# Performance work log

Hardware: AMD Instinct MI355X
Metric: run time of the kernel (lower is better)

Reference implementation:

```python
import jax, jax.numpy as jnp
import numpy as np

K_SPLINE = 3
GRID_N = 3
NUM_BASIS = GRID_N + K_SPLINE  # 6 coefficients per spline edge


def _make_grid(in_dim):
    # pykan-style uniform grid on [-1, 1] extended by k knots each side
    h = 2.0 / GRID_N
    g = -1.0 + h * jnp.arange(-K_SPLINE, GRID_N + K_SPLINE + 1, dtype=jnp.float32)
    return jnp.broadcast_to(g, (in_dim, g.shape[0]))  # [in, G+2k+1]


def _b_splines(x, grid):
    # Cox-de Boor recursion. x: [N, in], grid: [in, G+2k+1] -> [N, in, G+k]
    x = x[:, :, None]
    g = grid[None, :, :]
    B = ((x >= g[:, :, :-1]) & (x < g[:, :, 1:])).astype(x.dtype)
    for p in range(1, K_SPLINE + 1):
        B = ((x - g[:, :, :-(p + 1)]) / (g[:, :, p:-1] - g[:, :, :-(p + 1)]) * B[:, :, :-1]
             + (g[:, :, p + 1:] - x) / (g[:, :, p + 1:] - g[:, :, 1:-p]) * B[:, :, 1:])
    return B


def _kan_layer(x, grid, coef, scale_base, scale_sp, bias):
    # KANLayer: out_j = sum_i scale_base[i,j]*silu(x_i) + scale_sp[i,j]*spline_ij(x_i) + bias_j
    B = _b_splines(x, grid)                              # [N, in, G+k]
    spline = jnp.einsum('nib,iob->nio', B, coef)         # [N, in, out]
    act = scale_base[None] * jax.nn.silu(x)[:, :, None] + scale_sp[None] * spline
    return act.sum(axis=1) + bias[None, :]


def _calculate_w(strain, params):
    # strain: [B, S, 3] -> W: [B, S, 1]
    s1, s2, s3 = strain[..., 0], strain[..., 1], strain[..., 2]
    # C = 2E + I with E = [[s1, s3/2], [s3/2, s2]]
    a = 2.0 * s1 + 1.0
    d = 2.0 * s2 + 1.0
    b = s3
    detC = a * d - b * b
    logJ = 0.5 * jnp.log(detC)                           # log(det(C)**0.5)
    # analytic eigvalsh of symmetric 2x2, ascending order; double-where keeps
    # gradients finite at the degenerate point (strain == 0, C == I)
    m = 0.5 * (a + d)
    h2 = 0.25 * (a - d) ** 2 + b * b
    r = jnp.where(h2 > 0, jnp.sqrt(jnp.where(h2 > 0, h2, 1.0)), 0.0)
    eigs = jnp.sqrt(jnp.stack([m - r, m + r], axis=-1))  # principal stretches [B,S,2]
    aux = detC ** (-1.0 / 6.0)                           # J**(-1/3)
    reg = eigs * aux[..., None]
    kan_in = jnp.concatenate([reg ** params['ki0'],
                              (logJ * params['ki1'])[..., None]], axis=-1)  # [B,S,3]
    Bn, Sn = kan_in.shape[0], kan_in.shape[1]
    flat = kan_in.reshape(Bn * Sn, 3)
    h = _kan_layer(flat, _make_grid(3), params['coef0'], params['sb0'], params['sp0'], params['b0'])
    out = _kan_layer(h, _make_grid(1), params['coef1'], params['sb1'], params['sp1'], params['b1'])
    return out.reshape(Bn, Sn, -1)


def _forward(strain, params):
    # grad of sum(W) wrt strain (grad_outputs = ones), minus the same grad at zero strain.
    gradW = jax.grad(lambda s: _calculate_w(s, params).sum())(strain)
    zeros = jnp.zeros((1, 1, 3), strain.dtype)           # grad at 0 is identical per element
    grad0 = jax.grad(lambda s: _calculate_w(s, params).sum())(zeros)
    return gradW - grad0


def setup_inputs() -> dict:
    key = jax.random.key(0)
    ks = jax.random.split(key, 4)
    B, S = 4096, 512
    strain = 0.1 * jax.random.uniform(ks[0], (B, S, 3), dtype=jnp.float32)
    coef0 = 0.1 * jax.random.normal(ks[1], (3, 1, NUM_BASIS), dtype=jnp.float32)
    coef1 = 0.1 * jax.random.normal(ks[2], (1, 1, NUM_BASIS), dtype=jnp.float32)
    return {
        'strain': strain,
        'coef0': coef0,
        'sb0': jnp.full((3, 1), 1.0 / np.sqrt(3.0), jnp.float32),
        'sp0': jnp.ones((3, 1), jnp.float32),
        'b0': jnp.zeros((1,), jnp.float32),
        'coef1': coef1,
        'sb1': jnp.ones((1, 1), jnp.float32),
        'sp1': jnp.ones((1, 1), jnp.float32),
        'b1': jnp.zeros((1,), jnp.float32),
        'ki0': jnp.asarray(1.37, jnp.float32),  # ki[0] = 1 + random()
        'ki1': jnp.asarray(1.0, jnp.float32),   # ki[-1] fixed to 1.0 in __init__
    }


def reference(strain, coef0, sb0, sp0, b0, coef1, sb1, sp1, b1, ki0, ki1):
    params = {'coef0': coef0, 'sb0': sb0, 'sp0': sp0, 'b0': b0,
              'coef1': coef1, 'sb1': sb1, 'sp1': sp1, 'b1': b1,
              'ki0': ki0, 'ki1': ki1}
    return _forward(strain, params)
```

## Files before the change

kernel.cpp:

```cpp
#include <hip/hip_runtime.h>
#include <math.h>

#define NB 6

struct Params {
    float sb0[3], sp0[3];
    float b0;
    float sb1, sp1;
    float ki0, ki1;
};

__device__ __forceinline__ float fexp2(float x) { return __builtin_amdgcn_exp2f(x); }
__device__ __forceinline__ float flog2(float x) { return __builtin_amdgcn_logf(x); }
__device__ __forceinline__ float frcp(float x)  { return __builtin_amdgcn_rcpf(x); }
__device__ __forceinline__ float frsq(float x)  { return __builtin_amdgcn_rsqf(x); }

__device__ __forceinline__ void spline_eval(float x, const float (*__restrict__ tab)[8],
                                            float& sp, float& dsp) {
    float u  = fmaf(x, 1.5f, 4.5f);
    float fi = floorf(u);
    float f  = u - fi;
    int   i  = (int)fi;
    float msk = (u >= 0.0f && u < 9.0f) ? 1.0f : 0.0f;
    i = i < 0 ? 0 : (i > 8 ? 8 : i);
    const float4 A  = *reinterpret_cast<const float4*>(&tab[i][0]);
    const float4 Bv = *reinterpret_cast<const float4*>(&tab[i][4]);
    sp  = msk * fmaf(fmaf(fmaf(A.w, f, A.z), f, A.y), f, A.x);
    dsp = msk * fmaf(fmaf(Bv.z, f, Bv.y), f, Bv.x);
}

__device__ __forceinline__ void silu_fd(float x, float& s, float& ds) {
    float e   = fexp2(-1.44269504f * x);
    float sig = frcp(1.0f + e);
    s  = x * sig;
    ds = sig * (1.0f + x * (1.0f - sig));
}

__device__ void grad_sample(float s1, float s2, float s3, const Params& P,
                            const float (*__restrict__ tab)[9][8], float g[3]) {
    float a   = fmaf(2.0f, s1, 1.0f);
    float d   = fmaf(2.0f, s2, 1.0f);
    float b   = s3;
    float m   = 0.5f * (a + d);
    float amd = a - d;
    float h2  = fmaf(0.25f * amd, amd, b * b);
    bool  pos = h2 > 0.0f;
    float irr = pos ? frsq(h2) : 0.0f;
    float r   = h2 * irr;
    float t1  = m - r, t2 = m + r;
    float invDet = frcp(t1 * t2);
    float invt1 = t2 * invDet, invt2 = t1 * invDet;
    float Lt1 = flog2(t1), Lt2 = flog2(t2);
    float k   = P.ki0;
    float x0  = fexp2(k * (Lt1 * (1.0f / 3.0f) - Lt2 * (1.0f / 6.0f)));
    float x1  = fexp2(k * (Lt2 * (1.0f / 3.0f) - Lt1 * (1.0f / 6.0f)));
    float x2  = P.ki1 * 0.34657359f * (Lt1 + Lt2);

    float xs[3] = {x0, x1, x2};
    float hacc  = P.b0;
    float gx[3];
#pragma unroll
    for (int i = 0; i < 3; ++i) {
        float sp, dsp;
        spline_eval(xs[i], tab[i], sp, dsp);
        float si, dsi; silu_fd(xs[i], si, dsi);
        hacc += P.sb0[i] * si + P.sp0[i] * sp;
        gx[i] = P.sb0[i] * dsi + P.sp0[i] * dsp;
    }
    float sp2, dsp2;
    spline_eval(hacc, tab[3], sp2, dsp2);
    float si2, dsi2; silu_fd(hacc, si2, dsi2);
    float dWdh = P.sb1 * dsi2 + P.sp1 * dsp2;

    float P0 = dWdh * gx[0] * x0 * k;
    float P1 = dWdh * gx[1] * x1 * k;
    float w2c = dWdh * gx[2];
    float A = 0.5f * P0 * invt1;
    float B = 0.5f * P1 * invt2;
    float C = invDet * (0.5f * P.ki1 * w2c - (P0 + P1) * (1.0f / 6.0f));
    float dr0 = 0.25f * amd * irr;
    float dr2 = b * irr;
    float ApB = A + B, BmA = B - A;
    float h05 = 0.5f * ApB;
    float gA = h05 + BmA * dr0 + C * d;
    float gD = h05 - BmA * dr0 + C * a;
    float gB = BmA * dr2 - 2.0f * b * C;
    g[0] = 2.0f * gA;
    g[1] = 2.0f * gD;
    g[2] = gB;
}

__global__ __launch_bounds__(256) void kan_grad(
        const float* __restrict__ strain, float* __restrict__ out, int n,
        const float* __restrict__ c0, const float* __restrict__ sb0,
        const float* __restrict__ sp0, const float* __restrict__ b0,
        const float* __restrict__ c1, const float* __restrict__ sb1,
        const float* __restrict__ sp1, const float* __restrict__ ki0,
        const float* __restrict__ ki1) {
    __shared__ float tab[4][9][8];
    __shared__ float g0s[3];

    const int t = threadIdx.x;
    if (t < 36) {
        int tbl = t / 9, cell = t % 9;
        const float* cp = (tbl < 3) ? (c0 + tbl * NB) : c1;
        float cv[4];
#pragma unroll
        for (int kk = 0; kk < 4; ++kk) {
            int j = cell + kk - 3;
            cv[kk] = (j >= 0 && j < NB) ? cp[j] : 0.0f;
        }
        const float c16 = 1.0f / 6.0f;
        float a0 = (cv[0] + 4.0f * cv[1] + cv[2]) * c16;
        float a1 = (cv[2] - cv[0]) * 0.5f;
        float a2 = (cv[0] - 2.0f * cv[1] + cv[2]) * 0.5f;
        float a3 = (cv[3] - cv[0] + 3.0f * (cv[1] - cv[2])) * c16;
        tab[tbl][cell][0] = a0;
        tab[tbl][cell][1] = a1;
        tab[tbl][cell][2] = a2;
        tab[tbl][cell][3] = a3;
        tab[tbl][cell][4] = 1.5f * a1;
        tab[tbl][cell][5] = 3.0f * a2;
        tab[tbl][cell][6] = 4.5f * a3;
        tab[tbl][cell][7] = 0.0f;
    }

    Params P;
#pragma unroll
    for (int i = 0; i < 3; ++i) { P.sb0[i] = sb0[i]; P.sp0[i] = sp0[i]; }
    P.b0 = b0[0];
    P.sb1 = sb1[0]; P.sp1 = sp1[0];
    P.ki0 = ki0[0]; P.ki1 = ki1[0];

    __syncthreads();
    if (t == 0) {
        float g0[3];
        grad_sample(0.0f, 0.0f, 0.0f, P, tab, g0);
        g0s[0] = g0[0]; g0s[1] = g0[1]; g0s[2] = g0[2];
    }
    __syncthreads();
    const float g00 = g0s[0], g01 = g0s[1], g02 = g0s[2];

    const int ngroups = (n + 3) >> 2;
    for (int gi = blockIdx.x * blockDim.x + threadIdx.x; gi < ngroups;
         gi += gridDim.x * blockDim.x) {
        int i0 = gi * 4;
        if (i0 + 4 <= n) {
            const float4* sp4 = reinterpret_cast<const float4*>(strain + (size_t)i0 * 3);
            float4 v0 = sp4[0], v1 = sp4[1], v2 = sp4[2];
            float in[12] = {v0.x, v0.y, v0.z, v0.w,
                            v1.x, v1.y, v1.z, v1.w,
                            v2.x, v2.y, v2.z, v2.w};
            float o[12];
#pragma unroll
            for (int kk = 0; kk < 4; ++kk) {
                float g[3];
                grad_sample(in[3 * kk], in[3 * kk + 1], in[3 * kk + 2], P, tab, g);
                o[3 * kk]     = g[0] - g00;
                o[3 * kk + 1] = g[1] - g01;
                o[3 * kk + 2] = g[2] - g02;
            }
            float4* op4 = reinterpret_cast<float4*>(out + (size_t)i0 * 3);
            op4[0] = make_float4(o[0], o[1], o[2],  o[3]);
            op4[1] = make_float4(o[4], o[5], o[6],  o[7]);
            op4[2] = make_float4(o[8], o[9], o[10], o[11]);
        } else {
            for (int i = i0; i < n; ++i) {
                float g[3];
                grad_sample(strain[3 * i], strain[3 * i + 1], strain[3 * i + 2], P,
                            tab, g);
                out[3 * i]     = g[0] - g00;
                out[3 * i + 1] = g[1] - g01;
                out[3 * i + 2] = g[2] - g02;
            }
        }
    }
}

extern "C" void kernel_launch(void* const* d_in, const int* in_sizes, int n_in,
                              void* d_out, int out_size, void* d_ws, size_t ws_size,
                              hipStream_t stream) {
    const float* strain = (const float*)d_in[0];
    const float* c0  = (const float*)d_in[1];
    const float* sb0 = (const float*)d_in[2];
    const float* sp0 = (const float*)d_in[3];
    const float* b0  = (const float*)d_in[4];
    const float* c1  = (const float*)d_in[5];
    const float* sb1 = (const float*)d_in[6];
    const float* sp1 = (const float*)d_in[7];
    const float* ki0 = (const float*)d_in[9];
    const float* ki1 = (const float*)d_in[10];

    int n = in_sizes[0] / 3;
    int ngroups = (n + 3) / 4;
    int block = 256;
    int grid = (ngroups + block - 1) / block;
    if (grid > 8192) grid = 8192;

    kan_grad<<<grid, block, 0, stream>>>(strain, (float*)d_out, n,
                                         c0, sb0, sp0, b0, c1, sb1, sp1, ki0, ki1);
}
```

Before: 21.03 us.

## Simplify gradient algebra, compact spline table, process eight samples per thread

Rewrites the eigenvalue and gradient chain in terms of s1-s2 and s1+s2, and precomputes the ki-derived constants once per thread, removing several multiplies. The spline table shrinks to one float4 per cell, with the derivative polynomial derived from the same coefficients, halving shared-memory reads. Each thread now handles eight samples with six vector loads and stores instead of four, raising memory-level parallelism but halving the thread count and increasing register pressure.

```diff
diff --git a/kernel.cpp b/kernel.cpp
--- a/kernel.cpp
+++ b/kernel.cpp
@@ -7,7 +7,9 @@
     float sb0[3], sp0[3];
     float b0;
     float sb1, sp1;
-    float ki0, ki1;
+    float k3, k6, kh;
+    float cL;
+    float ch;
 };
 
 __device__ __forceinline__ float fexp2(float x) { return __builtin_amdgcn_exp2f(x); }
@@ -15,46 +17,45 @@
 __device__ __forceinline__ float frcp(float x)  { return __builtin_amdgcn_rcpf(x); }
 __device__ __forceinline__ float frsq(float x)  { return __builtin_amdgcn_rsqf(x); }
 
-__device__ __forceinline__ void spline_eval(float x, const float (*__restrict__ tab)[8],
+__device__ __forceinline__ void spline_eval(float x, const float4* __restrict__ tab,
                                             float& sp, float& dsp) {
     float u  = fmaf(x, 1.5f, 4.5f);
     float fi = floorf(u);
     float f  = u - fi;
     int   i  = (int)fi;
-    float msk = (u >= 0.0f && u < 9.0f) ? 1.0f : 0.0f;
+    bool  in = (u >= 0.0f && u < 9.0f);
+    float msk  = in ? 1.0f : 0.0f;
+    float msk15 = in ? 1.5f : 0.0f;
     i = i < 0 ? 0 : (i > 8 ? 8 : i);
-    const float4 A  = *reinterpret_cast<const float4*>(&tab[i][0]);
-    const float4 Bv = *reinterpret_cast<const float4*>(&tab[i][4]);
-    sp  = msk * fmaf(fmaf(fmaf(A.w, f, A.z), f, A.y), f, A.x);
-    dsp = msk * fmaf(fmaf(Bv.z, f, Bv.y), f, Bv.x);
+    const float4 A = tab[i];
+    sp  = msk  * fmaf(fmaf(fmaf(A.w, f, A.z), f, A.y), f, A.x);
+    float a2z = A.z + A.z;
+    float f3  = 3.0f * f;
+    dsp = msk15 * fmaf(f, fmaf(f3, A.w, a2z), A.y);
 }
 
 __device__ __forceinline__ void silu_fd(float x, float& s, float& ds) {
     float e   = fexp2(-1.44269504f * x);
     float sig = frcp(1.0f + e);
     s  = x * sig;
-    ds = sig * (1.0f + x * (1.0f - sig));
+    ds = sig * fmaf(x, 1.0f - sig, 1.0f);
 }
 
 __device__ void grad_sample(float s1, float s2, float s3, const Params& P,
-                            const float (*__restrict__ tab)[9][8], float g[3]) {
-    float a   = fmaf(2.0f, s1, 1.0f);
-    float d   = fmaf(2.0f, s2, 1.0f);
+                            const float4 (*__restrict__ tab)[9], float g[3]) {
+    float q   = s1 - s2;
+    float m   = s1 + s2 + 1.0f;
     float b   = s3;
-    float m   = 0.5f * (a + d);
-    float amd = a - d;
-    float h2  = fmaf(0.25f * amd, amd, b * b);
-    bool  pos = h2 > 0.0f;
-    float irr = pos ? frsq(h2) : 0.0f;
+    float h2  = fmaf(q, q, b * b);
+    float irr = h2 > 0.0f ? frsq(h2) : 0.0f;
     float r   = h2 * irr;
     float t1  = m - r, t2 = m + r;
     float invDet = frcp(t1 * t2);
     float invt1 = t2 * invDet, invt2 = t1 * invDet;
     float Lt1 = flog2(t1), Lt2 = flog2(t2);
-    float k   = P.ki0;
-    float x0  = fexp2(k * (Lt1 * (1.0f / 3.0f) - Lt2 * (1.0f / 6.0f)));
-    float x1  = fexp2(k * (Lt2 * (1.0f / 3.0f) - Lt1 * (1.0f / 6.0f)));
-    float x2  = P.ki1 * 0.34657359f * (Lt1 + Lt2);
+    float x0  = fexp2(fmaf(Lt1, P.k3, -Lt2 * P.k6));
+    float x1  = fexp2(fmaf(Lt2, P.k3, -Lt1 * P.k6));
+    float x2  = (Lt1 + Lt2) * P.cL;
 
     float xs[3] = {x0, x1, x2};
     float hacc  = P.b0;
@@ -72,22 +73,18 @@
     float si2, dsi2; silu_fd(hacc, si2, dsi2);
     float dWdh = P.sb1 * dsi2 + P.sp1 * dsp2;
 
-    float P0 = dWdh * gx[0] * x0 * k;
-    float P1 = dWdh * gx[1] * x1 * k;
+    float P0 = dWdh * gx[0] * x0;
+    float P1 = dWdh * gx[1] * x1;
     float w2c = dWdh * gx[2];
-    float A = 0.5f * P0 * invt1;
-    float B = 0.5f * P1 * invt2;
-    float C = invDet * (0.5f * P.ki1 * w2c - (P0 + P1) * (1.0f / 6.0f));
-    float dr0 = 0.25f * amd * irr;
-    float dr2 = b * irr;
-    float ApB = A + B, BmA = B - A;
-    float h05 = 0.5f * ApB;
-    float gA = h05 + BmA * dr0 + C * d;
-    float gD = h05 - BmA * dr0 + C * a;
-    float gB = BmA * dr2 - 2.0f * b * C;
-    g[0] = 2.0f * gA;
-    g[1] = 2.0f * gD;
-    g[2] = gB;
+    float A = P.kh * P0 * invt1;
+    float B = P.kh * P1 * invt2;
+    float C = invDet * fmaf(-P.k6, P0 + P1, P.ch * w2c);
+    float u0 = (B - A) * irr;
+    float w  = fmaf(C, m, 0.5f * (A + B));
+    float t  = q * fmaf(0.5f, u0, -C);
+    g[0] = 2.0f * (w + t);
+    g[1] = 2.0f * (w - t);
+    g[2] = b * fmaf(-2.0f, C, u0);
 }
 
 __global__ __launch_bounds__(256) void kan_grad(
@@ -97,7 +94,7 @@
         const float* __restrict__ c1, const float* __restrict__ sb1,
         const float* __restrict__ sp1, const float* __restrict__ ki0,
         const float* __restrict__ ki1) {
-    __shared__ float tab[4][9][8];
+    __shared__ float4 tab[4][9];
     __shared__ float g0s[3];
 
     const int t = threadIdx.x;
@@ -115,14 +112,7 @@
         float a1 = (cv[2] - cv[0]) * 0.5f;
         float a2 = (cv[0] - 2.0f * cv[1] + cv[2]) * 0.5f;
         float a3 = (cv[3] - cv[0] + 3.0f * (cv[1] - cv[2])) * c16;
-        tab[tbl][cell][0] = a0;
-        tab[tbl][cell][1] = a1;
-        tab[tbl][cell][2] = a2;
-        tab[tbl][cell][3] = a3;
-        tab[tbl][cell][4] = 1.5f * a1;
-        tab[tbl][cell][5] = 3.0f * a2;
-        tab[tbl][cell][6] = 4.5f * a3;
-        tab[tbl][cell][7] = 0.0f;
+        tab[tbl][cell] = make_float4(a0, a1, a2, a3);
     }
 
     Params P;
@@ -130,7 +120,12 @@
     for (int i = 0; i < 3; ++i) { P.sb0[i] = sb0[i]; P.sp0[i] = sp0[i]; }
     P.b0 = b0[0];
     P.sb1 = sb1[0]; P.sp1 = sp1[0];
-    P.ki0 = ki0[0]; P.ki1 = ki1[0];
+    float k = ki0[0], l = ki1[0];
+    P.k3 = k * (1.0f / 3.0f);
+    P.k6 = k * (1.0f / 6.0f);
+    P.kh = k * 0.5f;
+    P.cL = l * 0.34657359f;
+    P.ch = l * 0.5f;
 
     __syncthreads();
     if (t == 0) {
@@ -141,19 +136,19 @@
     __syncthreads();
     const float g00 = g0s[0], g01 = g0s[1], g02 = g0s[2];
 
-    const int ngroups = (n + 3) >> 2;
+    const int ngroups = (n + 7) >> 3;
     for (int gi = blockIdx.x * blockDim.x + threadIdx.x; gi < ngroups;
          gi += gridDim.x * blockDim.x) {
-        int i0 = gi * 4;
-        if (i0 + 4 <= n) {
+        int i0 = gi * 8;
+        if (i0 + 8 <= n) {
             const float4* sp4 = reinterpret_cast<const float4*>(strain + (size_t)i0 * 3);
-            float4 v0 = sp4[0], v1 = sp4[1], v2 = sp4[2];
-            float in[12] = {v0.x, v0.y, v0.z, v0.w,
-                            v1.x, v1.y, v1.z, v1.w,
-                            v2.x, v2.y, v2.z, v2.w};
-            float o[12];
+            float4 v[6];
 #pragma unroll
-            for (int kk = 0; kk < 4; ++kk) {
+            for (int kk = 0; kk < 6; ++kk) v[kk] = sp4[kk];
+            const float* in = reinterpret_cast<const float*>(v);
+            float o[24];
+#pragma unroll
+            for (int kk = 0; kk < 8; ++kk) {
                 float g[3];
                 grad_sample(in[3 * kk], in[3 * kk + 1], in[3 * kk + 2], P, tab, g);
                 o[3 * kk]     = g[0] - g00;
@@ -161,9 +156,9 @@
                 o[3 * kk + 2] = g[2] - g02;
             }
             float4* op4 = reinterpret_cast<float4*>(out + (size_t)i0 * 3);
-            op4[0] = make_float4(o[0], o[1], o[2],  o[3]);
-            op4[1] = make_float4(o[4], o[5], o[6],  o[7]);
-            op4[2] = make_float4(o[8], o[9], o[10], o[11]);
+            const float4* ov = reinterpret_cast<const float4*>(o);
+#pragma unroll
+            for (int kk = 0; kk < 6; ++kk) op4[kk] = ov[kk];
         } else {
             for (int i = i0; i < n; ++i) {
                 float g[3];
@@ -192,7 +187,7 @@
     const float* ki1 = (const float*)d_in[10];
 
     int n = in_sizes[0] / 3;
-    int ngroups = (n + 3) / 4;
+    int ngroups = (n + 7) / 8;
     int block = 256;
     int grid = (ngroups + block - 1) / block;
     if (grid > 8192) grid = 8192;
```

Measured after the change: 21.30 us. About the same (+1.3%).
